# Optimization experiments

Measured on AMD Instinct MI355X. Metric: run time of the kernel, lower is better.

The kernel has to match this reference:

```python
import jax, jax.numpy as jnp
import numpy as np

B, N, D = 16, 8192, 384   # examples, sentences per example, embedding dim
KN = 16                   # neighbors per node (kNN degree)
K, H, STEPS = 8, 128, 3   # coin dim, hidden dim, walk steps


def setup_inputs() -> dict:
    key = jax.random.key(0)
    ks = jax.random.split(key, 12)
    s = 0.02
    return {
        "sent_embs": jax.random.normal(ks[0], (B, N, D), dtype=jnp.float32),
        "q_embs": jax.random.normal(ks[1], (B, D), dtype=jnp.float32),
        "neighbors": jax.random.randint(ks[2], (B, N, KN), 0, N, dtype=jnp.int32),
        # coin_net: Linear(2D->H), ReLU, Linear(H->K)
        "coin_w1": jax.random.normal(ks[3], (2 * D, H), dtype=jnp.float32) * s,
        "coin_b1": jnp.zeros((H,), dtype=jnp.float32),
        "coin_w2": jax.random.normal(ks[4], (H, K), dtype=jnp.float32) * s,
        "coin_b2": jnp.zeros((K,), dtype=jnp.float32),
        # path_net: Linear(D+K+D->H), ReLU, Linear(H->1)
        "path_w1": jax.random.normal(ks[5], (D + K + D, H), dtype=jnp.float32) * s,
        "path_b1": jnp.zeros((H,), dtype=jnp.float32),
        "path_w2": jax.random.normal(ks[6], (H, 1), dtype=jnp.float32) * s,
        "path_b2": jnp.zeros((1,), dtype=jnp.float32),
    }


def _mlp(x, w1, b1, w2, b2):
    return jax.nn.relu(x @ w1 + b1) @ w2 + b2


def _forward(sent_embs, q_embs, neighbors,
             coin_w1, coin_b1, coin_w2, coin_b2,
             path_w1, path_b1, path_w2, path_b2):
    b, n, d = sent_embs.shape
    k = coin_w2.shape[1]
    q_bcast = jnp.broadcast_to(q_embs[:, None, :], (b, n, d))

    # coin amplitudes per node: [B, N, K]
    amps = _mlp(jnp.concatenate([sent_embs, q_bcast], axis=-1),
                coin_w1, coin_b1, coin_w2, coin_b2)

    # initial uniform walk state: 1/sqrt(N*K)
    state = jnp.full((b, n, k), 1.0 / np.sqrt(n * k), dtype=sent_embs.dtype)

    # adjacency = self-loop + edges row -> neighbors[row]; A @ X == X + masked neighbor gather-sum
    valid = (neighbors >= 0) & (neighbors < n)           # [B, N, KN]
    safe_nbrs = jnp.where(valid, neighbors, 0)
    batch_idx = jnp.arange(b)[:, None, None]

    for _ in range(STEPS):
        ns = state * amps                                # coin step
        gathered = ns[batch_idx, safe_nbrs]              # [B, N, KN, K]
        gathered = jnp.where(valid[..., None], gathered, 0.0)
        ns = ns + gathered.sum(axis=2)                   # sparse.mm(A, ns)
        norm = jnp.linalg.norm(ns.reshape(b, -1), axis=1)[:, None, None]
        state = ns / jnp.where(norm > 0, norm, 1.0)      # renormalize (guard norm==0)

    path_in = jnp.concatenate([sent_embs, state, q_bcast], axis=-1)  # [B, N, D+K+D]
    logits = _mlp(path_in, path_w1, path_b1, path_w2, path_b2)[..., 0]  # [B, N]
    return logits


def reference(sent_embs, q_embs, neighbors,
              coin_w1, coin_b1, coin_w2, coin_b2,
              path_w1, path_b1, path_w2, path_b2):
    return _forward(sent_embs, q_embs, neighbors,
                    coin_w1, coin_b1, coin_w2, coin_b2,
                    path_w1, path_b1, path_w2, path_b2)
```

## Files before the change

kernel.cpp:

```cpp
#include <hip/hip_runtime.h>

#define B_SZ 16
#define N_SZ 8192
#define D_SZ 384
#define KN_SZ 16
#define K_SZ 8
#define H_SZ 128
#define M_TOTAL (B_SZ * N_SZ)
#define KSTEPS 12
#define MT64 (M_TOTAL / 64)
#define LDSA_STRIDE 400

typedef short short8 __attribute__((ext_vector_type(8)));
typedef short short4v __attribute__((ext_vector_type(4)));
typedef float floatx4 __attribute__((ext_vector_type(4)));

__device__ __forceinline__ unsigned short f2bf(float f) {
    unsigned u = __builtin_bit_cast(unsigned, f);
    u += 0x7FFFu + ((u >> 16) & 1u);
    return (unsigned short)(u >> 16);
}
__device__ __forceinline__ float bf2f(unsigned short b) {
    unsigned u = ((unsigned)b) << 16;
    return __builtin_bit_cast(float, u);
}

__global__ void prep_kernel(const float* __restrict__ q_embs,
                            const float* __restrict__ coin_w1,
                            const float* __restrict__ coin_b1,
                            const float* __restrict__ path_w1,
                            const float* __restrict__ path_b1,
                            unsigned short* __restrict__ wswz,
                            float* __restrict__ qcoin, float* __restrict__ qpath,
                            float* __restrict__ norms) {
    int blk = blockIdx.x;
    int t = threadIdx.x;
    if (blk < 384) {
        int f = blk * 256 + t;
        int j  = f & 7;
        int l  = (f >> 3) & 63;
        int ss = (f >> 9) % KSTEPS;
        int ct = f / (KSTEPS * 512);
        int k = ss * 32 + ((l >> 4) << 3) + j;
        int n = ct * 16 + (l & 15);
        float v = (n < H_SZ) ? coin_w1[k * H_SZ + n]
                             : path_w1[k * H_SZ + (n - H_SZ)];
        wswz[f] = f2bf(v);
    } else if (blk == 384) {
        if (t < B_SZ) norms[t] = 0.f;
    } else {
        int b = blk - 385;
        const float* q = q_embs + b * D_SZ;
        if (t < H_SZ) {
            float acc = coin_b1[t];
            for (int d = 0; d < D_SZ; d++)
                acc += q[d] * coin_w1[(D_SZ + d) * H_SZ + t];
            qcoin[b * H_SZ + t] = acc;
        } else if (t < 2 * H_SZ) {
            int h = t - H_SZ;
            float acc = path_b1[h];
            for (int d = 0; d < D_SZ; d++)
                acc += q[d] * path_w1[(D_SZ + K_SZ + d) * H_SZ + h];
            qpath[b * H_SZ + h] = acc;
        }
    }
}

__global__ __launch_bounds__(256)
void gemm_fused(const float* __restrict__ sent,
                const unsigned short* __restrict__ wswz,
                unsigned short* __restrict__ hcoinB,
                unsigned short* __restrict__ hpathB) {
    __shared__ short als[64 * LDSA_STRIDE];
    const int tid = threadIdx.x;
    const int wave = tid >> 6, lane = tid & 63;
    const int m_lane = lane & 15, quad = lane >> 4;
    const int mt = blockIdx.x;

    const float* abase = sent + (size_t)mt * 64 * D_SZ;
#pragma unroll
    for (int g = 0; g < 3; g++) {
        float4 v[8];
#pragma unroll
        for (int u = 0; u < 8; u++)
            v[u] = *(const float4*)(abase + (size_t)((g * 8 + u) * 256 + tid) * 4);
#pragma unroll
        for (int u = 0; u < 8; u++) {
            int e4 = (g * 8 + u) * 256 + tid;
            int row = e4 / 96;
            int c4  = e4 - row * 96;
            short4v sv;
            sv.x = (short)f2bf(v[u].x); sv.y = (short)f2bf(v[u].y);
            sv.z = (short)f2bf(v[u].z); sv.w = (short)f2bf(v[u].w);
            *(short4v*)&als[row * LDSA_STRIDE + c4 * 4] = sv;
        }
    }
    __syncthreads();

    const unsigned short* wbase = wswz + (size_t)wave * 4 * KSTEPS * 512 + lane * 8;
    floatx4 acc[4][4];
#pragma unroll
    for (int rt = 0; rt < 4; rt++)
#pragma unroll
        for (int c = 0; c < 4; c++) acc[rt][c] = (floatx4){0.f, 0.f, 0.f, 0.f};

#pragma unroll
    for (int s = 0; s < KSTEPS; s++) {
        short8 bf[4];
#pragma unroll
        for (int c = 0; c < 4; c++)
            bf[c] = *(const short8*)(wbase + (size_t)(c * KSTEPS + s) * 512);
        short8 af[4];
#pragma unroll
        for (int rt = 0; rt < 4; rt++)
            af[rt] = *(const short8*)&als[(rt * 16 + m_lane) * LDSA_STRIDE + s * 32 + quad * 8];
#pragma unroll
        for (int rt = 0; rt < 4; rt++)
#pragma unroll
            for (int c = 0; c < 4; c++)
                acc[rt][c] = __builtin_amdgcn_mfma_f32_16x16x32_bf16(af[rt], bf[c], acc[rt][c], 0, 0, 0);
    }

    unsigned short* dstbase = (wave < 2) ? hcoinB : hpathB;
    const int colw = (wave & 1) * 64;
#pragma unroll
    for (int rt = 0; rt < 4; rt++) {
        int mt16 = mt * 4 + rt;
#pragma unroll
        for (int c = 0; c < 4; c++) {
            int col = colw + c * 16 + m_lane;
            short4v sv;
            sv.x = (short)f2bf(acc[rt][c][0]); sv.y = (short)f2bf(acc[rt][c][1]);
            sv.z = (short)f2bf(acc[rt][c][2]); sv.w = (short)f2bf(acc[rt][c][3]);
            *(short4v*)(dstbase + (size_t)mt16 * 2048 + col * 16 + quad * 4) = sv;
        }
    }
}

__global__ __launch_bounds__(256)
void amps_init_kernel(const unsigned short* __restrict__ hcoinB,
                      const float* __restrict__ qcoin,
                      const float* __restrict__ coin_w2,
                      const float* __restrict__ coin_b2,
                      float* __restrict__ amps, float* __restrict__ z0) {
    __shared__ float w2s[H_SZ * K_SZ];
    __shared__ float qcs[H_SZ];
    const int tid = threadIdx.x;
    const int m = blockIdx.x * 256 + tid;
    const int b = (blockIdx.x * 256) >> 13;
    for (int i = tid; i < H_SZ * K_SZ; i += 256) w2s[i] = coin_w2[i];
    if (tid < H_SZ) qcs[tid] = qcoin[b * H_SZ + tid];
    __syncthreads();

    const unsigned short* hb = hcoinB + (size_t)(m >> 4) * 2048 + (m & 15);
    float acc[K_SZ];
#pragma unroll
    for (int j = 0; j < K_SZ; j++) acc[j] = coin_b2[j];

    for (int h = 0; h < H_SZ; h++) {
        float hv = bf2f(hb[h * 16]) + qcs[h];
        hv = hv > 0.f ? hv : 0.f;
        float4 wa = *(const float4*)&w2s[h * 8];
        float4 wb = *(const float4*)&w2s[h * 8 + 4];
        acc[0] += hv * wa.x; acc[1] += hv * wa.y; acc[2] += hv * wa.z; acc[3] += hv * wa.w;
        acc[4] += hv * wb.x; acc[5] += hv * wb.y; acc[6] += hv * wb.z; acc[7] += hv * wb.w;
    }
    const float c0 = 1.0f / 256.0f;
    float4 o0 = {acc[0], acc[1], acc[2], acc[3]};
    float4 o1 = {acc[4], acc[5], acc[6], acc[7]};
    *(float4*)(amps + (size_t)m * 8)     = o0;
    *(float4*)(amps + (size_t)m * 8 + 4) = o1;
    float4 s0 = {acc[0]*c0, acc[1]*c0, acc[2]*c0, acc[3]*c0};
    float4 s1 = {acc[4]*c0, acc[5]*c0, acc[6]*c0, acc[7]*c0};
    *(float4*)(z0 + (size_t)m * 8)     = s0;
    *(float4*)(z0 + (size_t)m * 8 + 4) = s1;
}

__global__ __launch_bounds__(256)
void walk_step(const float* __restrict__ z,
               const int* __restrict__ neighbors,
               const float* __restrict__ amps,
               float* __restrict__ outz,
               float* __restrict__ norms, int last) {
    const int g = blockIdx.x * 256 + threadIdx.x;
    const int m = g >> 1, half = g & 1;
    const int b = m >> 13;
    const size_t nbase = (size_t)b << 13;
    const int off = half * 4;

    float4 v = *(const float4*)(z + (size_t)m * 8 + off);
    int nbr[KN_SZ];
    const int4* nb4 = (const int4*)(neighbors + (size_t)m * KN_SZ);
#pragma unroll
    for (int i = 0; i < 4; i++) *(int4*)&nbr[i * 4] = nb4[i];
#pragma unroll
    for (int i = 0; i < KN_SZ; i++) {
        int nn = nbr[i];
        if (nn >= 0 && nn < N_SZ) {
            float4 gv = *(const float4*)(z + (nbase + nn) * 8 + off);
            v.x += gv.x; v.y += gv.y; v.z += gv.z; v.w += gv.w;
        }
    }
    if (!last) {
        float4 a = *(const float4*)(amps + (size_t)m * 8 + off);
        v.x *= a.x; v.y *= a.y; v.z *= a.z; v.w *= a.w;
        *(float4*)(outz + (size_t)m * 8 + off) = v;
    } else {
        *(float4*)(outz + (size_t)m * 8 + off) = v;
        float ss = v.x * v.x + v.y * v.y + v.z * v.z + v.w * v.w;
#pragma unroll
        for (int o = 32; o > 0; o >>= 1) ss += __shfl_down(ss, o);
        __shared__ float blocksum;
        if (threadIdx.x == 0) blocksum = 0.f;
        __syncthreads();
        if ((threadIdx.x & 63) == 0) atomicAdd(&blocksum, ss);
        __syncthreads();
        if (threadIdx.x == 0) atomicAdd(&norms[b], blocksum);
    }
}

__global__ __launch_bounds__(256)
void logits_kernel(const unsigned short* __restrict__ hpathB,
                   const float* __restrict__ qpath,
                   const float* __restrict__ u2,
                   const float* __restrict__ norms,
                   const float* __restrict__ path_w1,
                   const float* __restrict__ path_w2,
                   const float* __restrict__ path_b2,
                   float* __restrict__ out) {
    __shared__ float w1t[H_SZ * K_SZ];
    __shared__ float w2s[H_SZ];
    __shared__ float qps[H_SZ];
    const int tid = threadIdx.x;
    const int m = blockIdx.x * 256 + tid;
    const int b = (blockIdx.x * 256) >> 13;
    for (int i = tid; i < K_SZ * H_SZ; i += 256) {
        int h = i >> 3, j = i & 7;
        w1t[i] = path_w1[(D_SZ + j) * H_SZ + h];
    }
    if (tid < H_SZ) { w2s[tid] = path_w2[tid]; qps[tid] = qpath[b * H_SZ + tid]; }
    __syncthreads();

    float ssq = norms[b];
    float inv = ssq > 0.f ? rsqrtf(ssq) : 1.0f;
    float st[K_SZ];
    {
        float4 s0 = *(const float4*)(u2 + (size_t)m * 8);
        float4 s1 = *(const float4*)(u2 + (size_t)m * 8 + 4);
        st[0] = s0.x * inv; st[1] = s0.y * inv; st[2] = s0.z * inv; st[3] = s0.w * inv;
        st[4] = s1.x * inv; st[5] = s1.y * inv; st[6] = s1.z * inv; st[7] = s1.w * inv;
    }

    const unsigned short* hb = hpathB + (size_t)(m >> 4) * 2048 + (m & 15);
    float acc = path_b2[0];
    for (int h = 0; h < H_SZ; h++) {
        float hv = bf2f(hb[h * 16]) + qps[h];
        float4 wa = *(const float4*)&w1t[h * 8];
        float4 wb = *(const float4*)&w1t[h * 8 + 4];
        hv += st[0]*wa.x + st[1]*wa.y + st[2]*wa.z + st[3]*wa.w
            + st[4]*wb.x + st[5]*wb.y + st[6]*wb.z + st[7]*wb.w;
        hv = hv > 0.f ? hv : 0.f;
        acc += hv * w2s[h];
    }
    out[m] = acc;
}

extern "C" void kernel_launch(void* const* d_in, const int* in_sizes, int n_in,
                              void* d_out, int out_size, void* d_ws, size_t ws_size,
                              hipStream_t stream) {
    const float* sent      = (const float*)d_in[0];
    const float* q_embs    = (const float*)d_in[1];
    const int*   neighbors = (const int*)d_in[2];
    const float* coin_w1   = (const float*)d_in[3];
    const float* coin_b1   = (const float*)d_in[4];
    const float* coin_w2   = (const float*)d_in[5];
    const float* coin_b2   = (const float*)d_in[6];
    const float* path_w1   = (const float*)d_in[7];
    const float* path_b1   = (const float*)d_in[8];
    const float* path_w2   = (const float*)d_in[9];
    const float* path_b2   = (const float*)d_in[10];
    float* out = (float*)d_out;

    char* ws = (char*)d_ws;
    unsigned short* wswz = (unsigned short*)ws;
    float* qcoin = (float*)(ws + 196608);
    float* qpath = (float*)(ws + 196608 + 8192);
    float* norms = (float*)(ws + 196608 + 16384);
    unsigned short* hcoinB = (unsigned short*)(ws + 213248);
    unsigned short* hpathB = hcoinB + (size_t)M_TOTAL * H_SZ;
    float* amps = (float*)(ws + 213248 + 2ull * 33554432ull);
    float* zA   = amps + (size_t)M_TOTAL * K_SZ;
    float* zB   = zA   + (size_t)M_TOTAL * K_SZ;

    prep_kernel<<<401, 256, 0, stream>>>(q_embs, coin_w1, coin_b1, path_w1, path_b1,
                                         wswz, qcoin, qpath, norms);
    gemm_fused<<<MT64, 256, 0, stream>>>(sent, wswz, hcoinB, hpathB);
    amps_init_kernel<<<M_TOTAL / 256, 256, 0, stream>>>(hcoinB, qcoin, coin_w2, coin_b2, amps, zA);
    walk_step<<<2 * M_TOTAL / 256, 256, 0, stream>>>(zA, neighbors, amps, zB, norms, 0);
    walk_step<<<2 * M_TOTAL / 256, 256, 0, stream>>>(zB, neighbors, amps, zA, norms, 0);
    walk_step<<<2 * M_TOTAL / 256, 256, 0, stream>>>(zA, neighbors, amps, zB, norms, 1);
    logits_kernel<<<M_TOTAL / 256, 256, 0, stream>>>(hpathB, qpath, zB, norms,
                                                     path_w1, path_w2, path_b2, out);
}
```

Baseline: 415.5 us.

## Fuse coin MLP epilogue into GEMM and merge walk/logits into cooperative kernel

Computes the coin second layer (ReLU plus H->K projection) inside the GEMM epilogue through shared memory, so the bf16 coin hidden activations are never written to global memory and the amps_init kernel goes away. The three walk steps and the logits stage are merged into one cooperative-groups kernel with grid.sync between phases, which removes several kernel launches. The logits stage is split across two threads per row, and packed bf16 conversion instructions are used. The cost is a dependency on cooperative launch with 1024 resident blocks, plus the latency of grid-wide barriers.

```diff
diff --git a/kernel.cpp b/kernel.cpp
--- a/kernel.cpp
+++ b/kernel.cpp
@@ -1,4 +1,5 @@
 #include <hip/hip_runtime.h>
+#include <hip/hip_cooperative_groups.h>
 
 #define B_SZ 16
 #define N_SZ 8192
@@ -23,6 +24,11 @@
 __device__ __forceinline__ float bf2f(unsigned short b) {
     unsigned u = ((unsigned)b) << 16;
     return __builtin_bit_cast(float, u);
+}
+__device__ __forceinline__ unsigned pkbf(float a, float b) {
+    unsigned r;
+    asm("v_cvt_pk_bf16_f32 %0, %1, %2" : "=v"(r) : "v"(a), "v"(b));
+    return r;
 }
 
 __global__ void prep_kernel(const float* __restrict__ q_embs,
@@ -69,13 +75,18 @@
 __global__ __launch_bounds__(256)
 void gemm_fused(const float* __restrict__ sent,
                 const unsigned short* __restrict__ wswz,
-                unsigned short* __restrict__ hcoinB,
-                unsigned short* __restrict__ hpathB) {
-    __shared__ short als[64 * LDSA_STRIDE];
+                const float* __restrict__ qcoin,
+                const float* __restrict__ coin_w2,
+                const float* __restrict__ coin_b2,
+                unsigned short* __restrict__ hpathB,
+                float* __restrict__ amps,
+                float* __restrict__ z0) {
+    __shared__ __align__(16) short als[64 * LDSA_STRIDE];
     const int tid = threadIdx.x;
     const int wave = tid >> 6, lane = tid & 63;
     const int m_lane = lane & 15, quad = lane >> 4;
     const int mt = blockIdx.x;
+    const int b = mt >> 7;
 
     const float* abase = sent + (size_t)mt * 64 * D_SZ;
 #pragma unroll
@@ -89,10 +100,10 @@
             int e4 = (g * 8 + u) * 256 + tid;
             int row = e4 / 96;
             int c4  = e4 - row * 96;
-            short4v sv;
-            sv.x = (short)f2bf(v[u].x); sv.y = (short)f2bf(v[u].y);
-            sv.z = (short)f2bf(v[u].z); sv.w = (short)f2bf(v[u].w);
-            *(short4v*)&als[row * LDSA_STRIDE + c4 * 4] = sv;
+            int2 p;
+            p.x = (int)pkbf(v[u].x, v[u].y);
+            p.y = (int)pkbf(v[u].z, v[u].w);
+            *(int2*)&als[row * LDSA_STRIDE + c4 * 4] = p;
         }
     }
     __syncthreads();
@@ -121,67 +132,70 @@
                 acc[rt][c] = __builtin_amdgcn_mfma_f32_16x16x32_bf16(af[rt], bf[c], acc[rt][c], 0, 0, 0);
     }
 
-    unsigned short* dstbase = (wave < 2) ? hcoinB : hpathB;
-    const int colw = (wave & 1) * 64;
-#pragma unroll
-    for (int rt = 0; rt < 4; rt++) {
-        int mt16 = mt * 4 + rt;
-#pragma unroll
-        for (int c = 0; c < 4; c++) {
-            int col = colw + c * 16 + m_lane;
-            short4v sv;
-            sv.x = (short)f2bf(acc[rt][c][0]); sv.y = (short)f2bf(acc[rt][c][1]);
-            sv.z = (short)f2bf(acc[rt][c][2]); sv.w = (short)f2bf(acc[rt][c][3]);
-            *(short4v*)(dstbase + (size_t)mt16 * 2048 + col * 16 + quad * 4) = sv;
-        }
-    }
-}
-
-__global__ __launch_bounds__(256)
-void amps_init_kernel(const unsigned short* __restrict__ hcoinB,
-                      const float* __restrict__ qcoin,
-                      const float* __restrict__ coin_w2,
-                      const float* __restrict__ coin_b2,
-                      float* __restrict__ amps, float* __restrict__ z0) {
-    __shared__ float w2s[H_SZ * K_SZ];
-    __shared__ float qcs[H_SZ];
-    const int tid = threadIdx.x;
-    const int m = blockIdx.x * 256 + tid;
-    const int b = (blockIdx.x * 256) >> 13;
+    if (wave >= 2) {
+        const int colw = (wave & 1) * 64;
+#pragma unroll
+        for (int rt = 0; rt < 4; rt++) {
+            int mt16 = mt * 4 + rt;
+#pragma unroll
+            for (int c = 0; c < 4; c++) {
+                int col = colw + c * 16 + m_lane;
+                int2 p;
+                p.x = (int)pkbf(acc[rt][c][0], acc[rt][c][1]);
+                p.y = (int)pkbf(acc[rt][c][2], acc[rt][c][3]);
+                *(int2*)(hpathB + (size_t)mt16 * 2048 + col * 16 + quad * 4) = p;
+            }
+        }
+    }
+    __syncthreads();
+
+    float* hs  = (float*)als;
+    float* w2s = hs + 64 * 132;
+    if (wave < 2) {
+        const int colw = wave * 64;
+        float qc[4];
+#pragma unroll
+        for (int c = 0; c < 4; c++)
+            qc[c] = qcoin[b * H_SZ + colw + c * 16 + m_lane];
+#pragma unroll
+        for (int rt = 0; rt < 4; rt++)
+#pragma unroll
+            for (int c = 0; c < 4; c++) {
+                int colj = colw + c * 16 + m_lane;
+#pragma unroll
+                for (int j = 0; j < 4; j++) {
+                    int row = rt * 16 + quad * 4 + j;
+                    float hv = acc[rt][c][j] + qc[c];
+                    hs[row * 132 + colj] = hv > 0.f ? hv : 0.f;
+                }
+            }
+    }
     for (int i = tid; i < H_SZ * K_SZ; i += 256) w2s[i] = coin_w2[i];
-    if (tid < H_SZ) qcs[tid] = qcoin[b * H_SZ + tid];
     __syncthreads();
 
-    const unsigned short* hb = hcoinB + (size_t)(m >> 4) * 2048 + (m & 15);
-    float acc[K_SZ];
-#pragma unroll
-    for (int j = 0; j < K_SZ; j++) acc[j] = coin_b2[j];
-
-    for (int h = 0; h < H_SZ; h++) {
-        float hv = bf2f(hb[h * 16]) + qcs[h];
-        hv = hv > 0.f ? hv : 0.f;
-        float4 wa = *(const float4*)&w2s[h * 8];
-        float4 wb = *(const float4*)&w2s[h * 8 + 4];
-        acc[0] += hv * wa.x; acc[1] += hv * wa.y; acc[2] += hv * wa.z; acc[3] += hv * wa.w;
-        acc[4] += hv * wb.x; acc[5] += hv * wb.y; acc[6] += hv * wb.z; acc[7] += hv * wb.w;
-    }
-    const float c0 = 1.0f / 256.0f;
-    float4 o0 = {acc[0], acc[1], acc[2], acc[3]};
-    float4 o1 = {acc[4], acc[5], acc[6], acc[7]};
-    *(float4*)(amps + (size_t)m * 8)     = o0;
-    *(float4*)(amps + (size_t)m * 8 + 4) = o1;
-    float4 s0 = {acc[0]*c0, acc[1]*c0, acc[2]*c0, acc[3]*c0};
-    float4 s1 = {acc[4]*c0, acc[5]*c0, acc[6]*c0, acc[7]*c0};
-    *(float4*)(z0 + (size_t)m * 8)     = s0;
-    *(float4*)(z0 + (size_t)m * 8 + 4) = s1;
-}
-
-__global__ __launch_bounds__(256)
-void walk_step(const float* __restrict__ z,
-               const int* __restrict__ neighbors,
-               const float* __restrict__ amps,
-               float* __restrict__ outz,
-               float* __restrict__ norms, int last) {
+    {
+        const int r = tid >> 2;
+        const int kk = (tid & 3) * 2;
+        float a0 = coin_b2[kk], a1 = coin_b2[kk + 1];
+#pragma unroll 8
+        for (int c = 0; c < H_SZ; c++) {
+            float hv = hs[r * 132 + c];
+            float2 w = *(const float2*)&w2s[c * 8 + kk];
+            a0 += hv * w.x; a1 += hv * w.y;
+        }
+        const size_t m = (size_t)mt * 64 + r;
+        const float c0 = 1.0f / 256.0f;
+        *(float2*)(amps + m * 8 + kk) = make_float2(a0, a1);
+        *(float2*)(z0   + m * 8 + kk) = make_float2(a0 * c0, a1 * c0);
+    }
+}
+
+__device__ __forceinline__ void walk_phase(const float* __restrict__ z,
+                                           float* __restrict__ outz,
+                                           const int* __restrict__ neighbors,
+                                           const float* __restrict__ amps,
+                                           float* __restrict__ norms,
+                                           float* blocksum, int last) {
     const int g = blockIdx.x * 256 + threadIdx.x;
     const int m = g >> 1, half = g & 1;
     const int b = m >> 13;
@@ -210,59 +224,72 @@
         float ss = v.x * v.x + v.y * v.y + v.z * v.z + v.w * v.w;
 #pragma unroll
         for (int o = 32; o > 0; o >>= 1) ss += __shfl_down(ss, o);
-        __shared__ float blocksum;
-        if (threadIdx.x == 0) blocksum = 0.f;
+        if (threadIdx.x == 0) *blocksum = 0.f;
         __syncthreads();
-        if ((threadIdx.x & 63) == 0) atomicAdd(&blocksum, ss);
+        if ((threadIdx.x & 63) == 0) atomicAdd(blocksum, ss);
         __syncthreads();
-        if (threadIdx.x == 0) atomicAdd(&norms[b], blocksum);
-    }
-}
-
-__global__ __launch_bounds__(256)
-void logits_kernel(const unsigned short* __restrict__ hpathB,
-                   const float* __restrict__ qpath,
-                   const float* __restrict__ u2,
-                   const float* __restrict__ norms,
-                   const float* __restrict__ path_w1,
-                   const float* __restrict__ path_w2,
-                   const float* __restrict__ path_b2,
-                   float* __restrict__ out) {
+        if (threadIdx.x == 0) atomicAdd(&norms[b], *blocksum);
+    }
+}
+
+__global__ __launch_bounds__(256, 4)
+void mega_kernel(float* __restrict__ zA, float* __restrict__ zB,
+                 const int* __restrict__ neighbors,
+                 const float* __restrict__ amps,
+                 float* __restrict__ norms,
+                 const unsigned short* __restrict__ hpathB,
+                 const float* __restrict__ qpath,
+                 const float* __restrict__ path_w1,
+                 const float* __restrict__ path_w2,
+                 const float* __restrict__ path_b2,
+                 float* __restrict__ out) {
+    cooperative_groups::grid_group grid = cooperative_groups::this_grid();
     __shared__ float w1t[H_SZ * K_SZ];
-    __shared__ float w2s[H_SZ];
+    __shared__ float w2sp[H_SZ];
     __shared__ float qps[H_SZ];
+    __shared__ float blocksum;
     const int tid = threadIdx.x;
-    const int m = blockIdx.x * 256 + tid;
-    const int b = (blockIdx.x * 256) >> 13;
-    for (int i = tid; i < K_SZ * H_SZ; i += 256) {
+    const int mbase = blockIdx.x * 128;
+    const int b = mbase >> 13;
+
+    for (int i = tid; i < H_SZ * K_SZ; i += 256) {
         int h = i >> 3, j = i & 7;
         w1t[i] = path_w1[(D_SZ + j) * H_SZ + h];
     }
-    if (tid < H_SZ) { w2s[tid] = path_w2[tid]; qps[tid] = qpath[b * H_SZ + tid]; }
-    __syncthreads();
+    if (tid < H_SZ) { w2sp[tid] = path_w2[tid]; qps[tid] = qpath[b * H_SZ + tid]; }
+
+    walk_phase(zA, zB, neighbors, amps, norms, &blocksum, 0);
+    grid.sync();
+    walk_phase(zB, zA, neighbors, amps, norms, &blocksum, 0);
+    grid.sync();
+    walk_phase(zA, zB, neighbors, amps, norms, &blocksum, 1);
+    grid.sync();
 
     float ssq = norms[b];
     float inv = ssq > 0.f ? rsqrtf(ssq) : 1.0f;
+    const int m = mbase + (tid >> 1);
+    const int hh = tid & 1;
     float st[K_SZ];
     {
-        float4 s0 = *(const float4*)(u2 + (size_t)m * 8);
-        float4 s1 = *(const float4*)(u2 + (size_t)m * 8 + 4);
+        float4 s0 = *(const float4*)(zB + (size_t)m * 8);
+        float4 s1 = *(const float4*)(zB + (size_t)m * 8 + 4);
         st[0] = s0.x * inv; st[1] = s0.y * inv; st[2] = s0.z * inv; st[3] = s0.w * inv;
         st[4] = s1.x * inv; st[5] = s1.y * inv; st[6] = s1.z * inv; st[7] = s1.w * inv;
     }
-
     const unsigned short* hb = hpathB + (size_t)(m >> 4) * 2048 + (m & 15);
-    float acc = path_b2[0];
-    for (int h = 0; h < H_SZ; h++) {
+    float acc = hh ? 0.f : path_b2[0];
+    const int h0 = hh * 64;
+    for (int h = h0; h < h0 + 64; h++) {
         float hv = bf2f(hb[h * 16]) + qps[h];
         float4 wa = *(const float4*)&w1t[h * 8];
         float4 wb = *(const float4*)&w1t[h * 8 + 4];
         hv += st[0]*wa.x + st[1]*wa.y + st[2]*wa.z + st[3]*wa.w
             + st[4]*wb.x + st[5]*wb.y + st[6]*wb.z + st[7]*wb.w;
         hv = hv > 0.f ? hv : 0.f;
-        acc += hv * w2s[h];
-    }
-    out[m] = acc;
+        acc += hv * w2sp[h];
+    }
+    float other = __shfl_xor(acc, 1);
+    if (!hh) out[m] = acc + other;
 }
 
 extern "C" void kernel_launch(void* const* d_in, const int* in_sizes, int n_in,
@@ -284,21 +311,20 @@
     char* ws = (char*)d_ws;
     unsigned short* wswz = (unsigned short*)ws;
     float* qcoin = (float*)(ws + 196608);
-    float* qpath = (float*)(ws + 196608 + 8192);
-    float* norms = (float*)(ws + 196608 + 16384);
-    unsigned short* hcoinB = (unsigned short*)(ws + 213248);
-    unsigned short* hpathB = hcoinB + (size_t)M_TOTAL * H_SZ;
-    float* amps = (float*)(ws + 213248 + 2ull * 33554432ull);
-    float* zA   = amps + (size_t)M_TOTAL * K_SZ;
-    float* zB   = zA   + (size_t)M_TOTAL * K_SZ;
+    float* qpath = (float*)(ws + 204800);
+    float* norms = (float*)(ws + 212992);
+    unsigned short* hpathB = (unsigned short*)(ws + 213248);
+    float* amps = (float*)(ws + 33767680);
+    float* zA   = (float*)(ws + 37961984);
+    float* zB   = (float*)(ws + 42156288);
 
     prep_kernel<<<401, 256, 0, stream>>>(q_embs, coin_w1, coin_b1, path_w1, path_b1,
                                          wswz, qcoin, qpath, norms);
-    gemm_fused<<<MT64, 256, 0, stream>>>(sent, wswz, hcoinB, hpathB);
-    amps_init_kernel<<<M_TOTAL / 256, 256, 0, stream>>>(hcoinB, qcoin, coin_w2, coin_b2, amps, zA);
-    walk_step<<<2 * M_TOTAL / 256, 256, 0, stream>>>(zA, neighbors, amps, zB, norms, 0);
-    walk_step<<<2 * M_TOTAL / 256, 256, 0, stream>>>(zB, neighbors, amps, zA, norms, 0);
-    walk_step<<<2 * M_TOTAL / 256, 256, 0, stream>>>(zA, neighbors, amps, zB, norms, 1);
-    logits_kernel<<<M_TOTAL / 256, 256, 0, stream>>>(hpathB, qpath, zB, norms,
-                                                     path_w1, path_w2, path_b2, out);
-}
+    gemm_fused<<<MT64, 256, 0, stream>>>(sent, wswz, qcoin, coin_w2, coin_b2,
+                                         hpathB, amps, zA);
+    void* margs[] = { (void*)&zA, (void*)&zB, (void*)&neighbors, (void*)&amps,
+                      (void*)&norms, (void*)&hpathB, (void*)&qpath,
+                      (void*)&path_w1, (void*)&path_w2, (void*)&path_b2, (void*)&out };
+    hipLaunchCooperativeKernel((void*)mega_kernel, dim3(1024), dim3(256),
+                               margs, 0, stream);
+}
```

Result: slower. 744.7 us (+79.2%).
